# Performance work log

Measured on AMD Instinct MI355X. Metric: run time of the kernel, lower is better.

The kernel has to match this reference:

```python
import jax, jax.numpy as jnp
import numpy as np

N_FFT = 512
HOP = N_FFT // 4  # torch.stft default hop_length
TWO_PI = 2.0 * np.pi


def _stft_phase(x):
    """torch.stft(x, n_fft=512, return_complex=True) phase: center reflect-pad,
    rectangular window, onesided rfft. Returns [F, T'] with F = n_fft//2+1."""
    pad = N_FFT // 2
    xp = jnp.pad(x, (pad, pad), mode='reflect')
    n_frames = (xp.shape[0] - N_FFT) // HOP + 1
    idx = (np.arange(n_frames, dtype=np.int32)[:, None] * HOP
           + np.arange(N_FFT, dtype=np.int32)[None, :])
    frames = xp[idx]                      # [T', n_fft]
    spec = jnp.fft.rfft(frames, axis=-1)  # [T', F]
    return jnp.angle(spec).T              # [F, T']


def _anti_wrap(x):
    return jnp.abs(x - jnp.round(x / TWO_PI) * TWO_PI)


def _gd(p):
    # banded matmul with gd_matrix == out[f] = p[f-1] - p[f], out[0] = -p[0]
    return jnp.concatenate([-p[:1], p[:-1] - p[1:]], axis=0)


def _iaf(p):
    # banded matmul with iaf_matrix along time axis
    return jnp.concatenate([-p[:, :1], p[:, :-1] - p[:, 1:]], axis=1)


def setup_inputs() -> dict:
    key = jax.random.key(0)
    k1, k2 = jax.random.split(key)
    T = 4194304  # 2^22 samples (~262 s @ 16 kHz)
    yd = jax.random.normal(k1, (T,), dtype=jnp.float32)
    td = jax.random.normal(k2, (T,), dtype=jnp.float32)
    return {"yd": yd, "td": td}


def reference(yd, td):
    pr = _stft_phase(yd)  # [F, T']
    pg = _stft_phase(td)
    ip_loss = jnp.mean(_anti_wrap(pr - pg))
    gd_loss = jnp.mean(_anti_wrap(_gd(pr) - _gd(pg)))
    iaf_loss = jnp.mean(_anti_wrap(_iaf(pr) - _iaf(pg)))
    return (ip_loss, gd_loss, iaf_loss)
```

## Files before the change

### kernel.cpp

```cpp
#include <hip/hip_runtime.h>
#include <math.h>

#define HOP     128
#define NSLOTS  256
#define FPW     4
#define PI_F    3.14159265358979323846f
#define PI2_F   1.57079632679489661923f
#define K8      0.70710678118654752440f

#define LDS_FENCE() do { __asm__ volatile("" ::: "memory"); \
                         __builtin_amdgcn_wave_barrier(); } while (0)

struct cpx { float x, y; };
__device__ __forceinline__ cpx cadd(cpx a, cpx b){ return {a.x+b.x, a.y+b.y}; }
__device__ __forceinline__ cpx csub(cpx a, cpx b){ return {a.x-b.x, a.y-b.y}; }
__device__ __forceinline__ cpx cmul(cpx a, cpx b){
    return {fmaf(a.x,b.x,-a.y*b.y), fmaf(a.x,b.y, a.y*b.x)};
}
__device__ __forceinline__ cpx cmulc(cpx a, cpx b){
    return {fmaf(a.x,b.x, a.y*b.y), fmaf(a.y,b.x,-a.x*b.y)};
}

__device__ __forceinline__ float abs_angle(float re, float im) {
    float a = fabsf(im), b = fabsf(re);
    float mn = fminf(a, b), mx = fmaxf(a, b);
    float t = __fdividef(mn, fmaxf(mx, 1e-37f));
    float t2 = t * t;
    float p = fmaf(t2, -0.0117212f, 0.05265332f);
    p = fmaf(t2, p, -0.11643287f);
    p = fmaf(t2, p, 0.19354346f);
    p = fmaf(t2, p, -0.33262347f);
    p = fmaf(t2, p, 0.99997726f);
    float r = t * p;
    r = (a > b) ? (PI2_F - r) : r;
    r = (re < 0.f) ? (PI_F - r) : r;
    return r;
}

__device__ __forceinline__ void dft8(cpx v[8]) {
    cpx a0=cadd(v[0],v[4]), a1=cadd(v[1],v[5]), a2=cadd(v[2],v[6]), a3=cadd(v[3],v[7]);
    cpx b0=csub(v[0],v[4]), b1=csub(v[1],v[5]), b2=csub(v[2],v[6]), b3=csub(v[3],v[7]);
    b1 = cpx{K8*(b1.x+b1.y), K8*(b1.y-b1.x)};
    b2 = cpx{b2.y, -b2.x};
    b3 = cpx{K8*(b3.y-b3.x), -K8*(b3.x+b3.y)};
    cpx c0=cadd(a0,a2), c2=csub(a0,a2);
    cpx c1=cadd(a1,a3), c3=csub(a1,a3); c3 = cpx{c3.y, -c3.x};
    cpx d0=cadd(b0,b2), d2=csub(b0,b2);
    cpx d1=cadd(b1,b3), d3=csub(b1,b3); d3 = cpx{d3.y, -d3.x};
    v[0]=cadd(c0,c1); v[4]=csub(c0,c1);
    v[2]=cadd(c2,c3); v[6]=csub(c2,c3);
    v[1]=cadd(d0,d1); v[5]=csub(d0,d1);
    v[3]=cadd(d2,d3); v[7]=csub(d2,d3);
}

__global__ __launch_bounds__(256, 4) void phase_loss_kernel(
        const float* __restrict__ y, const float* __restrict__ g,
        float* __restrict__ acc, int* __restrict__ ticket,
        float* __restrict__ out, int T, int n_frames, float inv_count) {
    __shared__ float2 xch_all[4][512];
    __shared__ float2 tw2_tab[7][8];
    __shared__ float wsum[3][4];
    __shared__ int is_last;

    const int tid  = threadIdx.x;
    const int lane = tid & 63;
    const int wid  = tid >> 6;
    const int l8   = lane & 7;
    float2* xch = xch_all[wid];

    if (tid < 56) {
        const int k = (tid >> 3) + 1, l = tid & 7;
        float s, c;
        __sincosf(-(2.0f * PI_F / 64.0f) * (float)(l * k), &s, &c);
        tw2_tab[tid >> 3][l] = make_float2(c, s);
    }
    __syncthreads();

    cpx tw1[7];
    #pragma unroll
    for (int k = 1; k < 8; ++k) {
        float a1 = -(2.0f * PI_F / 512.0f) * (float)(lane * k);
        __sincosf(a1, &tw1[k - 1].y, &tw1[k - 1].x);
    }

    float ip = 0.f, gd = 0.f, iaf = 0.f;
    cpx Cp[5];
    const int tmax_int = (T - 256) / HOP;
    const int ra1 = (lane >> 3) * 72 + (lane & 7);
    const int ra2 = (lane >> 3) * 65 + (lane & 7) * 8;
    const int rsl = (lane + 63) & 63;
    const int rsh = (64 - lane) & 63;

    auto do_frame = [&](int t, bool accum, bool hp) {
        cpx v[8];
        const int base = t * HOP - 256 + lane;
        if (t >= 2 && t <= tmax_int) {
            #pragma unroll
            for (int r = 0; r < 8; ++r) {
                int j = base + r * 64;
                v[r].x = y[j]; v[r].y = g[j];
            }
        } else {
            #pragma unroll
            for (int r = 0; r < 8; ++r) {
                int j = base + r * 64;
                j = (j < 0) ? -j : j;
                j = (j >= T) ? (2 * T - 2 - j) : j;
                v[r].x = y[j]; v[r].y = g[j];
            }
        }
        dft8(v);
        #pragma unroll
        for (int k = 1; k < 8; ++k) v[k] = cmul(v[k], tw1[k - 1]);
        LDS_FENCE();
        #pragma unroll
        for (int k = 0; k < 8; ++k)
            xch[lane ^ (72 * k)] = make_float2(v[k].x, v[k].y);
        LDS_FENCE();
        #pragma unroll
        for (int r = 0; r < 8; ++r) {
            float2 tmp = xch[ra1 ^ (r << 3)];
            v[r] = cpx{tmp.x, tmp.y};
        }
        dft8(v);
        #pragma unroll
        for (int k = 1; k < 8; ++k) {
            float2 tw = tw2_tab[k - 1][l8];
            v[k] = cmul(v[k], cpx{tw.x, tw.y});
        }
        LDS_FENCE();
        #pragma unroll
        for (int k = 0; k < 8; ++k)
            xch[lane ^ (65 * k)] = make_float2(v[k].x, v[k].y);
        LDS_FENCE();
        #pragma unroll
        for (int r = 0; r < 8; ++r) {
            float2 tmp = xch[ra2 ^ r];
            v[r] = cpx{tmp.x, tmp.y};
        }
        dft8(v);
        cpx Cc[5];
        #pragma unroll
        for (int jj = 0; jj < 5; ++jj) {
            float px = __shfl(v[7 - jj].x, rsh, 64);
            float py = __shfl(v[7 - jj].y, rsh, 64);
            px = (lane == 0) ? v[(8 - jj) & 7].x : px;
            py = (lane == 0) ? v[(8 - jj) & 7].y : py;
            float ur = v[jj].x + px, ui = v[jj].y - py;
            float vx = v[jj].x - px, vy = v[jj].y + py;
            Cc[jj].x = fmaf(ur, vy, -ui * vx);
            Cc[jj].y = fmaf(ur, vx,  ui * vy);
        }
        if (accum) {
            cpx rprev = {0.f, 0.f};
            #pragma unroll
            for (int jj = 0; jj < 4; ++jj) {
                cpx rj;
                rj.x = __shfl(Cc[jj].x, rsl, 64);
                rj.y = __shfl(Cc[jj].y, rsl, 64);
                cpx cmj = (jj > 0 && lane == 0) ? rprev : rj;
                cpx cc = Cc[jj];
                float aw = abs_angle(cc.x, cc.y);
                ip += aw;
                cpx qg = cmulc(cmj, cc);
                float gt = abs_angle(qg.x, qg.y);
                gd += (jj == 0 && lane == 0) ? aw : gt;
                if (hp) {
                    cpx qi = cmulc(Cp[jj], cc);
                    iaf += abs_angle(qi.x, qi.y);
                } else {
                    iaf += aw;
                }
                rprev = rj;
            }
            if (lane == 0) {
                cpx cc = Cc[4];
                float aw = abs_angle(cc.x, cc.y);
                ip += aw;
                cpx qg = cmulc(rprev, cc);
                gd += abs_angle(qg.x, qg.y);
                if (hp) {
                    cpx qi = cmulc(Cp[4], cc);
                    iaf += abs_angle(qi.x, qi.y);
                } else {
                    iaf += aw;
                }
            }
        }
        #pragma unroll
        for (int jj = 0; jj < 5; ++jj) Cp[jj] = Cc[jj];
    };

    const int chain   = (blockIdx.x << 2) | wid;
    const int nchains = (int)(gridDim.x << 2);
    const int t0 = chain * FPW;
    int tend = t0 + FPW;
    if (chain == nchains - 1) tend = n_frames;
    const bool havep = (t0 > 0);

    if (havep) do_frame(t0 - 1, false, false);
    #pragma unroll 2
    for (int t = t0; t < tend; ++t)
        do_frame(t, true, havep || (t > t0));

    __syncthreads();
    for (int off = 32; off; off >>= 1) {
        ip  += __shfl_down(ip, off);
        gd  += __shfl_down(gd, off);
        iaf += __shfl_down(iaf, off);
    }
    if (lane == 0) { wsum[0][wid] = ip; wsum[1][wid] = gd; wsum[2][wid] = iaf; }
    __syncthreads();
    if (tid == 0) {
        const int slot = (int)(blockIdx.x & (NSLOTS - 1));
        atomicAdd(acc + 0 * NSLOTS + slot, wsum[0][0] + wsum[0][1] + wsum[0][2] + wsum[0][3]);
        atomicAdd(acc + 1 * NSLOTS + slot, wsum[1][0] + wsum[1][1] + wsum[1][2] + wsum[1][3]);
        atomicAdd(acc + 2 * NSLOTS + slot, wsum[2][0] + wsum[2][1] + wsum[2][2] + wsum[2][3]);
        __threadfence();
        is_last = (atomicAdd(ticket, 1) == (int)gridDim.x - 1);
    }
    __syncthreads();
    if (is_last) {
        for (int l = 0; l < 3; l++) {
            float vv = __hip_atomic_load(acc + l * NSLOTS + tid,
                                         __ATOMIC_RELAXED, __HIP_MEMORY_SCOPE_AGENT);
            for (int off = 32; off; off >>= 1) vv += __shfl_down(vv, off);
            if (lane == 0) wsum[l][wid] = vv;
        }
        __syncthreads();
        if (tid < 3)
            out[tid] = (wsum[tid][0] + wsum[tid][1] + wsum[tid][2] + wsum[tid][3]) * inv_count;
    }
}

extern "C" void kernel_launch(void* const* d_in, const int* in_sizes, int n_in,
                              void* d_out, int out_size, void* d_ws, size_t ws_size,
                              hipStream_t stream) {
    const float* y = (const float*)d_in[0];
    const float* g = (const float*)d_in[1];
    float* out = (float*)d_out;
    float* acc = (float*)d_ws;
    int* ticket = (int*)((char*)d_ws + 3 * NSLOTS * sizeof(float));
    const int T = in_sizes[0];
    const int n_frames = T / HOP + 1;
    int n_blocks = n_frames / (FPW * 4);
    if (n_blocks < 1) n_blocks = 1;

    hipMemsetAsync(d_ws, 0, 3 * NSLOTS * sizeof(float) + sizeof(int), stream);
    const float inv_count = 1.0f / (257.0f * (float)n_frames);
    phase_loss_kernel<<<n_blocks, 256, 0, stream>>>(y, g, acc, ticket, out,
                                                    T, n_frames, inv_count);
}
```

Before: 144.4 us.

## Switch to single-wave blocks, one frame chain per block

Each block now holds a single 64-lane wave that processes one chain of frames, instead of four waves per block. This removes the block-wide __syncthreads barriers and the cross-wave LDS reduction, and replaces the table setup barrier with a wave-level fence. The cost is four times as many blocks, so four times as many global atomics and ticket increments, plus more per-block setup of twiddle tables.

```diff
diff --git a/kernel.cpp b/kernel.cpp
--- a/kernel.cpp
+++ b/kernel.cpp
@@ -53,28 +53,24 @@
     v[3]=cadd(d2,d3); v[7]=csub(d2,d3);
 }
 
-__global__ __launch_bounds__(256, 4) void phase_loss_kernel(
+__global__ __launch_bounds__(64, 4) void phase_loss_kernel(
         const float* __restrict__ y, const float* __restrict__ g,
         float* __restrict__ acc, int* __restrict__ ticket,
         float* __restrict__ out, int T, int n_frames, float inv_count) {
-    __shared__ float2 xch_all[4][512];
+    __shared__ float2 xch[512];
     __shared__ float2 tw2_tab[7][8];
-    __shared__ float wsum[3][4];
     __shared__ int is_last;
 
-    const int tid  = threadIdx.x;
-    const int lane = tid & 63;
-    const int wid  = tid >> 6;
+    const int lane = threadIdx.x;
     const int l8   = lane & 7;
-    float2* xch = xch_all[wid];
-
-    if (tid < 56) {
-        const int k = (tid >> 3) + 1, l = tid & 7;
+
+    if (lane < 56) {
+        const int k = (lane >> 3) + 1, l = lane & 7;
         float s, c;
         __sincosf(-(2.0f * PI_F / 64.0f) * (float)(l * k), &s, &c);
-        tw2_tab[tid >> 3][l] = make_float2(c, s);
-    }
-    __syncthreads();
+        tw2_tab[lane >> 3][l] = make_float2(c, s);
+    }
+    LDS_FENCE();
 
     cpx tw1[7];
     #pragma unroll
@@ -191,11 +187,10 @@
         for (int jj = 0; jj < 5; ++jj) Cp[jj] = Cc[jj];
     };
 
-    const int chain   = (blockIdx.x << 2) | wid;
-    const int nchains = (int)(gridDim.x << 2);
+    const int chain = (int)blockIdx.x;
     const int t0 = chain * FPW;
     int tend = t0 + FPW;
-    if (chain == nchains - 1) tend = n_frames;
+    if (chain == (int)gridDim.x - 1) tend = n_frames;
     const bool havep = (t0 > 0);
 
     if (havep) do_frame(t0 - 1, false, false);
@@ -203,33 +198,31 @@
     for (int t = t0; t < tend; ++t)
         do_frame(t, true, havep || (t > t0));
 
-    __syncthreads();
     for (int off = 32; off; off >>= 1) {
         ip  += __shfl_down(ip, off);
         gd  += __shfl_down(gd, off);
         iaf += __shfl_down(iaf, off);
     }
-    if (lane == 0) { wsum[0][wid] = ip; wsum[1][wid] = gd; wsum[2][wid] = iaf; }
-    __syncthreads();
-    if (tid == 0) {
+    if (lane == 0) {
         const int slot = (int)(blockIdx.x & (NSLOTS - 1));
-        atomicAdd(acc + 0 * NSLOTS + slot, wsum[0][0] + wsum[0][1] + wsum[0][2] + wsum[0][3]);
-        atomicAdd(acc + 1 * NSLOTS + slot, wsum[1][0] + wsum[1][1] + wsum[1][2] + wsum[1][3]);
-        atomicAdd(acc + 2 * NSLOTS + slot, wsum[2][0] + wsum[2][1] + wsum[2][2] + wsum[2][3]);
+        atomicAdd(acc + 0 * NSLOTS + slot, ip);
+        atomicAdd(acc + 1 * NSLOTS + slot, gd);
+        atomicAdd(acc + 2 * NSLOTS + slot, iaf);
         __threadfence();
         is_last = (atomicAdd(ticket, 1) == (int)gridDim.x - 1);
     }
     __syncthreads();
     if (is_last) {
+        #pragma unroll
         for (int l = 0; l < 3; l++) {
-            float vv = __hip_atomic_load(acc + l * NSLOTS + tid,
-                                         __ATOMIC_RELAXED, __HIP_MEMORY_SCOPE_AGENT);
+            float vv = 0.f;
+            #pragma unroll
+            for (int k = 0; k < 4; ++k)
+                vv += __hip_atomic_load(acc + l * NSLOTS + lane + (k << 6),
+                                        __ATOMIC_RELAXED, __HIP_MEMORY_SCOPE_AGENT);
             for (int off = 32; off; off >>= 1) vv += __shfl_down(vv, off);
-            if (lane == 0) wsum[l][wid] = vv;
-        }
-        __syncthreads();
-        if (tid < 3)
-            out[tid] = (wsum[tid][0] + wsum[tid][1] + wsum[tid][2] + wsum[tid][3]) * inv_count;
+            if (lane == 0) out[l] = vv * inv_count;
+        }
     }
 }
 
@@ -243,11 +236,11 @@
     int* ticket = (int*)((char*)d_ws + 3 * NSLOTS * sizeof(float));
     const int T = in_sizes[0];
     const int n_frames = T / HOP + 1;
-    int n_blocks = n_frames / (FPW * 4);
+    int n_blocks = n_frames / FPW;
     if (n_blocks < 1) n_blocks = 1;
 
     hipMemsetAsync(d_ws, 0, 3 * NSLOTS * sizeof(float) + sizeof(int), stream);
     const float inv_count = 1.0f / (257.0f * (float)n_frames);
-    phase_loss_kernel<<<n_blocks, 256, 0, stream>>>(y, g, acc, ticket, out,
-                                                    T, n_frames, inv_count);
-}
+    phase_loss_kernel<<<n_blocks, 64, 0, stream>>>(y, g, acc, ticket, out,
+                                                   T, n_frames, inv_count);
+}
```

After: 276.5 us. 91.5% more time.
